# Kernel optimization log

Measured on AMD Instinct MI355X. Metric: run time of the kernel, lower is better.

## Reference

```python
import jax, jax.numpy as jnp
import numpy as np

B, S, D = 4, 4096, 2048
DFF = 4 * D
SKIP = 0.125


def setup_inputs() -> dict:
    key = jax.random.key(0)
    ks = jax.random.split(key, 4)
    s_in = 1.0 / np.sqrt(D).astype(np.float32)
    s_ff = 1.0 / np.sqrt(DFF).astype(np.float32)
    return {
        "x": jax.random.normal(ks[0], (B, S, D), jnp.float32),
        "Wr": jax.random.normal(ks[1], (D, 1), jnp.float32) * s_in,
        "br": jnp.zeros((1,), jnp.float32),
        "W1": jax.random.normal(ks[2], (D, DFF), jnp.float32) * s_in,
        "b1": jnp.zeros((DFF,), jnp.float32),
        "W2": jax.random.normal(ks[3], (DFF, D), jnp.float32) * s_ff,
        "b2": jnp.zeros((D,), jnp.float32),
    }


def reference(x, Wr, br, W1, b1, W2, b2):
    Bs, Ss, Ds = x.shape
    k = max(int(Ss * SKIP), 1)
    # Router: tiny linear D -> 1
    logits = (x @ Wr + br)[..., 0]                      # [B, S]
    # Top-k token selection along sequence
    weights, idx = jax.lax.top_k(logits, k)             # [B, k] (unsorted order within topk)
    perm = jnp.argsort(idx, axis=1)                     # torch.sort's sort-indices
    tokens = jnp.take_along_axis(idx, perm, axis=1)     # sorted token positions [B, k]
    # Gather selected tokens
    fx = jnp.take_along_axis(x, tokens[..., None], axis=1)  # [B, k, D]
    h = jax.nn.gelu(fx @ W1 + b1, approximate=False)    # [B, k, 4D]
    out_l = h @ W2 + b2                                  # [B, k, D]
    # Softmax over topk router logits, reordered to sorted-token order
    tw = jax.nn.softmax(weights, axis=1)                # [B, k]
    rw = jnp.take_along_axis(tw, perm, axis=1)          # [B, k]
    xw = rw[..., None] * out_l                           # [B, k, D]
    # scatter_add back onto x at the selected token positions
    bidx = jnp.arange(Bs)[:, None]                       # [B, 1]
    return x.at[bidx, tokens].add(xw)
```

## Files before the change

kernel.cpp:

```cpp
#include <hip/hip_runtime.h>
#include <math.h>

#define B_DIM   4
#define S_DIM   4096
#define D_DIM   2048
#define DFF_DIM 8192
#define K_TOP   512
#define M_ROWS  (B_DIM * K_TOP)
#define NSPLIT  4

typedef _Float16 half8 __attribute__((ext_vector_type(8)));
typedef _Float16 half4 __attribute__((ext_vector_type(4)));
typedef float    floatx4 __attribute__((ext_vector_type(4)));

static const size_t OFF_LOGITS = 0;
static const size_t OFF_TOK    = 65536;
static const size_t OFF_RW     = 73728;
static const size_t OFF_FX     = 81920;
static const size_t OFF_W1T    = OFF_FX  + (size_t)M_ROWS * D_DIM * 2;
static const size_t OFF_W2T    = OFF_W1T + (size_t)DFF_DIM * D_DIM * 2;
static const size_t OFF_H      = OFF_W2T + (size_t)D_DIM * DFF_DIM * 2;
static const size_t WS_NEEDED  = OFF_H   + (size_t)M_ROWS * DFF_DIM * 2;
static const size_t OFF_PART   = OFF_W1T;

__device__ __forceinline__ void async_ld16(const void* g, void* l) {
  __builtin_amdgcn_global_load_lds((const __attribute__((address_space(1))) unsigned int*)g,
                                   (__attribute__((address_space(3))) unsigned int*)l,
                                   16, 0, 0);
}

__global__ __launch_bounds__(256) void router_logits(const float* __restrict__ x,
                                                     const float* __restrict__ Wr,
                                                     const float* __restrict__ br,
                                                     float* __restrict__ logits) {
  int row  = blockIdx.x * 4 + (threadIdx.x >> 6);
  int lane = threadIdx.x & 63;
  const float4* xr = (const float4*)(x + (size_t)row * D_DIM);
  const float4* wr = (const float4*)Wr;
  float s = 0.f;
#pragma unroll
  for (int i = 0; i < (D_DIM / 4) / 64; ++i) {
    float4 a = xr[lane + i * 64];
    float4 w = wr[lane + i * 64];
    s += a.x * w.x + a.y * w.y + a.z * w.z + a.w * w.w;
  }
#pragma unroll
  for (int off = 32; off > 0; off >>= 1) s += __shfl_down(s, off, 64);
  if (lane == 0) logits[row] = s + br[0];
}

__global__ __launch_bounds__(256) void topk_select(const float* __restrict__ logits,
                                                   int* __restrict__ tokens,
                                                   float* __restrict__ rw) {
  int b = blockIdx.x;
  const float* lg = logits + (size_t)b * S_DIM;
  __shared__ unsigned int keys[S_DIM];
  __shared__ unsigned int bins[256];
  __shared__ unsigned int sscan[256];
  __shared__ unsigned int sh_prefix, sh_r;
  __shared__ float sel_logit[K_TOP];
  __shared__ float red[8];

  int tid = threadIdx.x;
  for (int s = tid; s < S_DIM; s += 256) {
    unsigned int u = __float_as_uint(lg[s]);
    keys[s] = (u & 0x80000000u) ? ~u : (u | 0x80000000u);
  }
  if (tid == 0) { sh_prefix = 0u; sh_r = K_TOP; }
  __syncthreads();

  for (int p = 24; p >= 0; p -= 8) {
    bins[tid] = 0u;
    __syncthreads();
    unsigned int prefix = sh_prefix;
    unsigned int maskhi = (p == 24) ? 0u : (0xFFFFFFFFu << (p + 8));
    for (int s = tid; s < S_DIM; s += 256) {
      unsigned int kk = keys[s];
      if ((kk & maskhi) == prefix) atomicAdd(&bins[(kk >> p) & 255u], 1u);
    }
    __syncthreads();
    sscan[tid] = bins[255 - tid];
    __syncthreads();
#pragma unroll
    for (int off = 1; off < 256; off <<= 1) {
      unsigned int v = (tid >= off) ? sscan[tid - off] : 0u;
      __syncthreads();
      sscan[tid] += v;
      __syncthreads();
    }
    unsigned int r = sh_r;
    unsigned int above = (tid > 0) ? sscan[tid - 1] : 0u;
    bool hit = (sscan[tid] >= r) && (above < r);
    __syncthreads();
    if (hit) {
      sh_prefix = prefix | ((unsigned int)(255 - tid) << p);
      sh_r = r - above;
    }
    __syncthreads();
  }
  unsigned int T = sh_prefix;

  int s0 = tid * 16;
  unsigned int g = 0, e = 0;
#pragma unroll
  for (int j = 0; j < 16; ++j) {
    unsigned int kk = keys[s0 + j];
    g += (kk > T);
    e += (kk == T);
  }
  sscan[tid] = g | (e << 16);
  __syncthreads();
#pragma unroll
  for (int off = 1; off < 256; off <<= 1) {
    unsigned int v = (tid >= off) ? sscan[tid - off] : 0u;
    __syncthreads();
    sscan[tid] += v;
    __syncthreads();
  }
  unsigned int incl = sscan[tid];
  unsigned int Gtot = sscan[255] & 0xFFFFu;
  unsigned int need = (unsigned int)K_TOP - Gtot;
  unsigned int gr = (incl & 0xFFFFu) - g;
  unsigned int er = (incl >> 16) - e;
#pragma unroll
  for (int j = 0; j < 16; ++j) {
    unsigned int kk = keys[s0 + j];
    if (kk > T) {
      unsigned int pos = gr + (er < need ? er : need);
      tokens[b * K_TOP + (int)pos] = s0 + j;
      sel_logit[pos] = __uint_as_float((kk & 0x80000000u) ? (kk & 0x7FFFFFFFu) : ~kk);
      gr++;
    } else if (kk == T) {
      if (er < need) {
        unsigned int pos = gr + er;
        tokens[b * K_TOP + (int)pos] = s0 + j;
        sel_logit[pos] = __uint_as_float((kk & 0x80000000u) ? (kk & 0x7FFFFFFFu) : ~kk);
      }
      er++;
    }
  }
  __syncthreads();

  int lane = tid & 63, wv = tid >> 6;
  float mx = -1e30f;
  for (int i = tid; i < K_TOP; i += 256) mx = fmaxf(mx, sel_logit[i]);
#pragma unroll
  for (int off = 32; off > 0; off >>= 1) mx = fmaxf(mx, __shfl_down(mx, off, 64));
  if (lane == 0) red[wv] = mx;
  __syncthreads();
  if (tid == 0) red[0] = fmaxf(fmaxf(red[0], red[1]), fmaxf(red[2], red[3]));
  __syncthreads();
  float M = red[0];
  float sm = 0.f;
  for (int i = tid; i < K_TOP; i += 256) sm += expf(sel_logit[i] - M);
#pragma unroll
  for (int off = 32; off > 0; off >>= 1) sm += __shfl_down(sm, off, 64);
  if (lane == 0) red[4 + wv] = sm;
  __syncthreads();
  if (tid == 0) red[4] = red[4] + red[5] + red[6] + red[7];
  __syncthreads();
  float SUM = red[4];
  for (int i = tid; i < K_TOP; i += 256) rw[b * K_TOP + i] = expf(sel_logit[i] - M) / SUM;
}

__global__ __launch_bounds__(256) void transpose_cvt(const float* __restrict__ in,
                                                     _Float16* __restrict__ out,
                                                     int K, int N) {
  __shared__ float tile[64][65];
  int nb = blockIdx.x * 64, kb = blockIdx.y * 64;
  int tid = threadIdx.x;
  int lr = tid >> 4;
  int lc = (tid & 15) * 4;
#pragma unroll
  for (int p = 0; p < 4; ++p) {
    int row = p * 16 + lr;
    float4 v = *(const float4*)(in + (size_t)(kb + row) * N + nb + lc);
    tile[row][lc] = v.x; tile[row][lc + 1] = v.y; tile[row][lc + 2] = v.z; tile[row][lc + 3] = v.w;
  }
  __syncthreads();
#pragma unroll
  for (int p = 0; p < 2; ++p) {
    int cc = p * 256 + tid;
    int n  = cc >> 3;
    int kc = (cc & 7) * 8;
    half8 o;
#pragma unroll
    for (int j = 0; j < 8; ++j) o[j] = (_Float16)tile[kc + j][n];
    *(half8*)(out + (size_t)(nb + n) * K + kb + kc) = o;
  }
}

__global__ __launch_bounds__(256) void gather_cvt(const float* __restrict__ x,
                                                  const int* __restrict__ tokens,
                                                  _Float16* __restrict__ fx) {
  int row = blockIdx.x;
  int b = row >> 9;
  int token = tokens[row];
  const float4* src = (const float4*)(x + ((size_t)b * S_DIM + token) * D_DIM);
  half4* dst = (half4*)(fx + (size_t)row * D_DIM);
  for (int i = threadIdx.x; i < D_DIM / 4; i += 256) {
    float4 v = src[i];
    half4 o;
    o[0] = (_Float16)v.x; o[1] = (_Float16)v.y; o[2] = (_Float16)v.z; o[3] = (_Float16)v.w;
    dst[i] = o;
  }
}

template <int EPI>
__global__ __launch_bounds__(256) void gemm_bt(const _Float16* __restrict__ A,
                                               const _Float16* __restrict__ Bt,
                                               const float* __restrict__ bias,
                                               _Float16* __restrict__ Co,
                                               int M, int N, int K, int Kspan) {
  __shared__ _Float16 As[128 * 32];
  __shared__ _Float16 Bs[128 * 32];
  const int tid = threadIdx.x;
  const int lane = tid & 63;
  const int wave = tid >> 6;
  const int bm = blockIdx.y * 128;
  const int bn = blockIdx.x * 128;
  const int wm = (wave & 1) * 64;
  const int wn = (wave >> 1) * 64;
  const int mr = lane & 15;
  const int sw = (((lane >> 4) ^ ((lane >> 1) & 3))) * 8;
  const int k0 = blockIdx.z * Kspan;

  floatx4 acc[4][4] = {};

  for (int kt = k0; kt < k0 + Kspan; kt += 32) {
#pragma unroll
    for (int j = 0; j < 2; ++j) {
      int c = (wave * 2 + j) * 64 + lane;
      int m  = c >> 2;
      int g  = (c & 3) ^ ((m >> 1) & 3);
      async_ld16(A  + (size_t)(bm + m) * K + kt + g * 8, As + (size_t)(wave * 2 + j) * 512);
      async_ld16(Bt + (size_t)(bn + m) * K + kt + g * 8, Bs + (size_t)(wave * 2 + j) * 512);
    }
    __syncthreads();

    half8 af[4], bf[4];
#pragma unroll
    for (int i = 0; i < 4; ++i) af[i] = *(const half8*)(As + (wm + i * 16 + mr) * 32 + sw);
#pragma unroll
    for (int j = 0; j < 4; ++j) bf[j] = *(const half8*)(Bs + (wn + j * 16 + mr) * 32 + sw);
#pragma unroll
    for (int i = 0; i < 4; ++i)
#pragma unroll
      for (int j = 0; j < 4; ++j)
        acc[i][j] = __builtin_amdgcn_mfma_f32_16x16x32_f16(af[i], bf[j], acc[i][j], 0, 0, 0);
    __syncthreads();
  }

  const int r0 = (lane >> 4) * 4;
  const int cn = lane & 15;
  if (EPI == 0) {
#pragma unroll
    for (int i = 0; i < 4; ++i)
#pragma unroll
      for (int j = 0; j < 4; ++j) {
        int col = bn + wn + j * 16 + cn;
        float bv = bias[col];
#pragma unroll
        for (int r = 0; r < 4; ++r) {
          int row = bm + wm + i * 16 + r0 + r;
          float v = acc[i][j][r] + bv;
          v = 0.5f * v * (1.0f + erff(v * 0.7071067811865475f));
          Co[(size_t)row * N + col] = (_Float16)v;
        }
      }
  } else {
    size_t zoff = (size_t)blockIdx.z * M;
#pragma unroll
    for (int i = 0; i < 4; ++i)
#pragma unroll
      for (int j = 0; j < 4; ++j) {
        int col = bn + wn + j * 16 + cn;
#pragma unroll
        for (int r = 0; r < 4; ++r) {
          int row = bm + wm + i * 16 + r0 + r;
          Co[(zoff + row) * N + col] = (_Float16)acc[i][j][r];
        }
      }
  }
}

__global__ __launch_bounds__(256) void reduce_scatter(const _Float16* __restrict__ part,
                                                      const float* __restrict__ bias,
                                                      const int* __restrict__ tokens,
                                                      const float* __restrict__ rw,
                                                      float* __restrict__ out) {
  int m = blockIdx.x;
  int b = m >> 9;
  int token = tokens[m];
  float wgt = rw[m];
  float* orow = out + ((size_t)b * S_DIM + token) * D_DIM;
  int c = threadIdx.x * 8;
  float acc[8] = {0, 0, 0, 0, 0, 0, 0, 0};
#pragma unroll
  for (int kz = 0; kz < NSPLIT; ++kz) {
    half8 p = *(const half8*)(part + ((size_t)kz * M_ROWS + m) * D_DIM + c);
#pragma unroll
    for (int j = 0; j < 8; ++j) acc[j] += (float)p[j];
  }
  float4 o0 = *(const float4*)(orow + c);
  float4 o1 = *(const float4*)(orow + c + 4);
  float4 b0 = *(const float4*)(bias + c);
  float4 b1 = *(const float4*)(bias + c + 4);
  o0.x += wgt * (acc[0] + b0.x);
  o0.y += wgt * (acc[1] + b0.y);
  o0.z += wgt * (acc[2] + b0.z);
  o0.w += wgt * (acc[3] + b0.w);
  o1.x += wgt * (acc[4] + b1.x);
  o1.y += wgt * (acc[5] + b1.y);
  o1.z += wgt * (acc[6] + b1.z);
  o1.w += wgt * (acc[7] + b1.w);
  *(float4*)(orow + c)     = o0;
  *(float4*)(orow + c + 4) = o1;
}

extern "C" void kernel_launch(void* const* d_in, const int* in_sizes, int n_in,
                              void* d_out, int out_size, void* d_ws, size_t ws_size,
                              hipStream_t stream) {
  const float* x  = (const float*)d_in[0];
  const float* Wr = (const float*)d_in[1];
  const float* br = (const float*)d_in[2];
  const float* W1 = (const float*)d_in[3];
  const float* b1 = (const float*)d_in[4];
  const float* W2 = (const float*)d_in[5];
  const float* b2 = (const float*)d_in[6];
  float* out = (float*)d_out;

  if (ws_size < WS_NEEDED) return;

  char* ws = (char*)d_ws;
  float*     logits = (float*)(ws + OFF_LOGITS);
  int*       tokens = (int*)(ws + OFF_TOK);
  float*     rw     = (float*)(ws + OFF_RW);
  _Float16*  fx     = (_Float16*)(ws + OFF_FX);
  _Float16*  W1T    = (_Float16*)(ws + OFF_W1T);
  _Float16*  W2T    = (_Float16*)(ws + OFF_W2T);
  _Float16*  h      = (_Float16*)(ws + OFF_H);
  _Float16*  part   = (_Float16*)(ws + OFF_PART);

  hipMemcpyAsync(out, x, (size_t)B_DIM * S_DIM * D_DIM * sizeof(float),
                 hipMemcpyDeviceToDevice, stream);

  transpose_cvt<<<dim3(DFF_DIM / 64, D_DIM / 64), 256, 0, stream>>>(W1, W1T, D_DIM, DFF_DIM);
  transpose_cvt<<<dim3(D_DIM / 64, DFF_DIM / 64), 256, 0, stream>>>(W2, W2T, DFF_DIM, D_DIM);

  router_logits<<<(B_DIM * S_DIM) / 4, 256, 0, stream>>>(x, Wr, br, logits);
  topk_select<<<B_DIM, 256, 0, stream>>>(logits, tokens, rw);
  gather_cvt<<<M_ROWS, 256, 0, stream>>>(x, tokens, fx);

  gemm_bt<0><<<dim3(DFF_DIM / 128, M_ROWS / 128, 1), 256, 0, stream>>>(
      fx, W1T, b1, h, M_ROWS, DFF_DIM, D_DIM, D_DIM);
  gemm_bt<2><<<dim3(D_DIM / 128, M_ROWS / 128, NSPLIT), 256, 0, stream>>>(
      h, W2T, nullptr, part, M_ROWS, D_DIM, DFF_DIM, DFF_DIM / NSPLIT);
  reduce_scatter<<<M_ROWS, 256, 0, stream>>>(part, b2, tokens, rw, out);
}
```

Measured before the change: 625.6 us.

## Double-buffer GEMM LDS tiles and fuse output copy with scatter-add

The GEMM main loop now uses two LDS buffers with manual s_waitcnt and barriers, so the asynchronous global-to-LDS loads for the next K-tile run while MFMAs consume the current one. The device-to-device memcpy of x into the output and the separate scatter kernel are replaced by one finalize kernel over all tokens. It copies x and, for selected tokens found through a new selmap, adds the weighted FFN result. That selmap reuses the logits workspace region, so it depends on topk_select reading each logit before overwriting it, and the hand-coded waitcnt masks must match the hardware encoding.

```diff
diff --git a/kernel.cpp b/kernel.cpp
--- a/kernel.cpp
+++ b/kernel.cpp
@@ -14,6 +14,7 @@
 typedef float    floatx4 __attribute__((ext_vector_type(4)));
 
 static const size_t OFF_LOGITS = 0;
+static const size_t OFF_SELMAP = 0;
 static const size_t OFF_TOK    = 65536;
 static const size_t OFF_RW     = 73728;
 static const size_t OFF_FX     = 81920;
@@ -28,6 +29,10 @@
                                    (__attribute__((address_space(3))) unsigned int*)l,
                                    16, 0, 0);
 }
+
+#define WAITCNT_VM4   0x0F74
+#define WAITCNT_VM0   0x0F70
+#define WAITCNT_LGKM0 0xC07F
 
 __global__ __launch_bounds__(256) void router_logits(const float* __restrict__ x,
                                                      const float* __restrict__ Wr,
@@ -49,7 +54,8 @@
   if (lane == 0) logits[row] = s + br[0];
 }
 
-__global__ __launch_bounds__(256) void topk_select(const float* __restrict__ logits,
+__global__ __launch_bounds__(256) void topk_select(const float* logits,
+                                                   int* selmap,
                                                    int* __restrict__ tokens,
                                                    float* __restrict__ rw) {
   int b = blockIdx.x;
@@ -65,6 +71,7 @@
   for (int s = tid; s < S_DIM; s += 256) {
     unsigned int u = __float_as_uint(lg[s]);
     keys[s] = (u & 0x80000000u) ? ~u : (u | 0x80000000u);
+    selmap[b * S_DIM + s] = -1;
   }
   if (tid == 0) { sh_prefix = 0u; sh_r = K_TOP; }
   __syncthreads();
@@ -129,12 +136,14 @@
       unsigned int pos = gr + (er < need ? er : need);
       tokens[b * K_TOP + (int)pos] = s0 + j;
       sel_logit[pos] = __uint_as_float((kk & 0x80000000u) ? (kk & 0x7FFFFFFFu) : ~kk);
+      selmap[b * S_DIM + s0 + j] = (int)pos;
       gr++;
     } else if (kk == T) {
       if (er < need) {
         unsigned int pos = gr + er;
         tokens[b * K_TOP + (int)pos] = s0 + j;
         sel_logit[pos] = __uint_as_float((kk & 0x80000000u) ? (kk & 0x7FFFFFFFu) : ~kk);
+        selmap[b * S_DIM + s0 + j] = (int)pos;
       }
       er++;
     }
@@ -212,8 +221,8 @@
                                                const float* __restrict__ bias,
                                                _Float16* __restrict__ Co,
                                                int M, int N, int K, int Kspan) {
-  __shared__ _Float16 As[128 * 32];
-  __shared__ _Float16 Bs[128 * 32];
+  __shared__ _Float16 As[2][128 * 32];
+  __shared__ _Float16 Bs[2][128 * 32];
   const int tid = threadIdx.x;
   const int lane = tid & 63;
   const int wave = tid >> 6;
@@ -222,33 +231,78 @@
   const int wm = (wave & 1) * 64;
   const int wn = (wave >> 1) * 64;
   const int mr = lane & 15;
-  const int sw = (((lane >> 4) ^ ((lane >> 1) & 3))) * 8;
+  const int sw = ((lane >> 4) ^ ((lane >> 1) & 3)) * 8;
   const int k0 = blockIdx.z * Kspan;
+  const int kend = k0 + Kspan;
+
+  const int c0 = (wave * 2) * 64 + lane;
+  const int c1 = (wave * 2 + 1) * 64 + lane;
+  const int m0 = c0 >> 2, g0 = (c0 & 3) ^ ((m0 >> 1) & 3);
+  const int m1 = c1 >> 2, g1 = (c1 & 3) ^ ((m1 >> 1) & 3);
+  const _Float16* a0p = A  + (size_t)(bm + m0) * K + g0 * 8;
+  const _Float16* a1p = A  + (size_t)(bm + m1) * K + g1 * 8;
+  const _Float16* b0p = Bt + (size_t)(bn + m0) * K + g0 * 8;
+  const _Float16* b1p = Bt + (size_t)(bn + m1) * K + g1 * 8;
+  const int slot0 = (wave * 2) * 512;
+  const int slot1 = (wave * 2 + 1) * 512;
 
   floatx4 acc[4][4] = {};
 
-  for (int kt = k0; kt < k0 + Kspan; kt += 32) {
-#pragma unroll
-    for (int j = 0; j < 2; ++j) {
-      int c = (wave * 2 + j) * 64 + lane;
-      int m  = c >> 2;
-      int g  = (c & 3) ^ ((m >> 1) & 3);
-      async_ld16(A  + (size_t)(bm + m) * K + kt + g * 8, As + (size_t)(wave * 2 + j) * 512);
-      async_ld16(Bt + (size_t)(bn + m) * K + kt + g * 8, Bs + (size_t)(wave * 2 + j) * 512);
-    }
-    __syncthreads();
-
-    half8 af[4], bf[4];
-#pragma unroll
-    for (int i = 0; i < 4; ++i) af[i] = *(const half8*)(As + (wm + i * 16 + mr) * 32 + sw);
-#pragma unroll
-    for (int j = 0; j < 4; ++j) bf[j] = *(const half8*)(Bs + (wn + j * 16 + mr) * 32 + sw);
-#pragma unroll
-    for (int i = 0; i < 4; ++i)
-#pragma unroll
-      for (int j = 0; j < 4; ++j)
-        acc[i][j] = __builtin_amdgcn_mfma_f32_16x16x32_f16(af[i], bf[j], acc[i][j], 0, 0, 0);
-    __syncthreads();
+  async_ld16(a0p + k0, &As[0][slot0]);
+  async_ld16(b0p + k0, &Bs[0][slot0]);
+  async_ld16(a1p + k0, &As[0][slot1]);
+  async_ld16(b1p + k0, &Bs[0][slot1]);
+
+  for (int kt = k0; kt < kend; kt += 64) {
+    {
+      int kn = kt + 32;
+      async_ld16(a0p + kn, &As[1][slot0]);
+      async_ld16(b0p + kn, &Bs[1][slot0]);
+      async_ld16(a1p + kn, &As[1][slot1]);
+      async_ld16(b1p + kn, &Bs[1][slot1]);
+      __builtin_amdgcn_s_waitcnt(WAITCNT_VM4);
+    }
+    __builtin_amdgcn_s_barrier();
+    {
+      half8 af[4], bf[4];
+#pragma unroll
+      for (int i = 0; i < 4; ++i) af[i] = *(const half8*)(&As[0][(wm + i * 16 + mr) * 32 + sw]);
+#pragma unroll
+      for (int j = 0; j < 4; ++j) bf[j] = *(const half8*)(&Bs[0][(wn + j * 16 + mr) * 32 + sw]);
+#pragma unroll
+      for (int i = 0; i < 4; ++i)
+#pragma unroll
+        for (int j = 0; j < 4; ++j)
+          acc[i][j] = __builtin_amdgcn_mfma_f32_16x16x32_f16(af[i], bf[j], acc[i][j], 0, 0, 0);
+    }
+    __builtin_amdgcn_s_waitcnt(WAITCNT_LGKM0);
+    __builtin_amdgcn_s_barrier();
+
+    if (kt + 64 < kend) {
+      int kn = kt + 64;
+      async_ld16(a0p + kn, &As[0][slot0]);
+      async_ld16(b0p + kn, &Bs[0][slot0]);
+      async_ld16(a1p + kn, &As[0][slot1]);
+      async_ld16(b1p + kn, &Bs[0][slot1]);
+      __builtin_amdgcn_s_waitcnt(WAITCNT_VM4);
+    } else {
+      __builtin_amdgcn_s_waitcnt(WAITCNT_VM0);
+    }
+    __builtin_amdgcn_s_barrier();
+    {
+      half8 af[4], bf[4];
+#pragma unroll
+      for (int i = 0; i < 4; ++i) af[i] = *(const half8*)(&As[1][(wm + i * 16 + mr) * 32 + sw]);
+#pragma unroll
+      for (int j = 0; j < 4; ++j) bf[j] = *(const half8*)(&Bs[1][(wn + j * 16 + mr) * 32 + sw]);
+#pragma unroll
+      for (int i = 0; i < 4; ++i)
+#pragma unroll
+        for (int j = 0; j < 4; ++j)
+          acc[i][j] = __builtin_amdgcn_mfma_f32_16x16x32_f16(af[i], bf[j], acc[i][j], 0, 0, 0);
+    }
+    __builtin_amdgcn_s_waitcnt(WAITCNT_LGKM0);
+    __builtin_amdgcn_s_barrier();
   }
 
   const int r0 = (lane >> 4) * 4;
@@ -284,38 +338,40 @@
   }
 }
 
-__global__ __launch_bounds__(256) void reduce_scatter(const _Float16* __restrict__ part,
-                                                      const float* __restrict__ bias,
-                                                      const int* __restrict__ tokens,
-                                                      const float* __restrict__ rw,
-                                                      float* __restrict__ out) {
-  int m = blockIdx.x;
-  int b = m >> 9;
-  int token = tokens[m];
-  float wgt = rw[m];
-  float* orow = out + ((size_t)b * S_DIM + token) * D_DIM;
+__global__ __launch_bounds__(256) void finalize(const float* __restrict__ x,
+                                                const _Float16* __restrict__ part,
+                                                const float* __restrict__ bias,
+                                                const int* __restrict__ selmap,
+                                                const float* __restrict__ rw,
+                                                float* __restrict__ out) {
+  int row = blockIdx.x;
+  size_t base = (size_t)row * D_DIM;
+  int sel = selmap[row];
   int c = threadIdx.x * 8;
-  float acc[8] = {0, 0, 0, 0, 0, 0, 0, 0};
-#pragma unroll
-  for (int kz = 0; kz < NSPLIT; ++kz) {
-    half8 p = *(const half8*)(part + ((size_t)kz * M_ROWS + m) * D_DIM + c);
-#pragma unroll
-    for (int j = 0; j < 8; ++j) acc[j] += (float)p[j];
-  }
-  float4 o0 = *(const float4*)(orow + c);
-  float4 o1 = *(const float4*)(orow + c + 4);
-  float4 b0 = *(const float4*)(bias + c);
-  float4 b1 = *(const float4*)(bias + c + 4);
-  o0.x += wgt * (acc[0] + b0.x);
-  o0.y += wgt * (acc[1] + b0.y);
-  o0.z += wgt * (acc[2] + b0.z);
-  o0.w += wgt * (acc[3] + b0.w);
-  o1.x += wgt * (acc[4] + b1.x);
-  o1.y += wgt * (acc[5] + b1.y);
-  o1.z += wgt * (acc[6] + b1.z);
-  o1.w += wgt * (acc[7] + b1.w);
-  *(float4*)(orow + c)     = o0;
-  *(float4*)(orow + c + 4) = o1;
+  float4 o0 = *(const float4*)(x + base + c);
+  float4 o1 = *(const float4*)(x + base + c + 4);
+  if (sel >= 0) {
+    float wgt = rw[sel];
+    float acc[8] = {0, 0, 0, 0, 0, 0, 0, 0};
+#pragma unroll
+    for (int kz = 0; kz < NSPLIT; ++kz) {
+      half8 p = *(const half8*)(part + ((size_t)kz * M_ROWS + sel) * D_DIM + c);
+#pragma unroll
+      for (int j = 0; j < 8; ++j) acc[j] += (float)p[j];
+    }
+    float4 b0 = *(const float4*)(bias + c);
+    float4 b1 = *(const float4*)(bias + c + 4);
+    o0.x += wgt * (acc[0] + b0.x);
+    o0.y += wgt * (acc[1] + b0.y);
+    o0.z += wgt * (acc[2] + b0.z);
+    o0.w += wgt * (acc[3] + b0.w);
+    o1.x += wgt * (acc[4] + b1.x);
+    o1.y += wgt * (acc[5] + b1.y);
+    o1.z += wgt * (acc[6] + b1.z);
+    o1.w += wgt * (acc[7] + b1.w);
+  }
+  *(float4*)(out + base + c)     = o0;
+  *(float4*)(out + base + c + 4) = o1;
 }
 
 extern "C" void kernel_launch(void* const* d_in, const int* in_sizes, int n_in,
@@ -334,6 +390,7 @@
 
   char* ws = (char*)d_ws;
   float*     logits = (float*)(ws + OFF_LOGITS);
+  int*       selmap = (int*)(ws + OFF_SELMAP);
   int*       tokens = (int*)(ws + OFF_TOK);
   float*     rw     = (float*)(ws + OFF_RW);
   _Float16*  fx     = (_Float16*)(ws + OFF_FX);
@@ -342,19 +399,16 @@
   _Float16*  h      = (_Float16*)(ws + OFF_H);
   _Float16*  part   = (_Float16*)(ws + OFF_PART);
 
-  hipMemcpyAsync(out, x, (size_t)B_DIM * S_DIM * D_DIM * sizeof(float),
-                 hipMemcpyDeviceToDevice, stream);
-
   transpose_cvt<<<dim3(DFF_DIM / 64, D_DIM / 64), 256, 0, stream>>>(W1, W1T, D_DIM, DFF_DIM);
   transpose_cvt<<<dim3(D_DIM / 64, DFF_DIM / 64), 256, 0, stream>>>(W2, W2T, DFF_DIM, D_DIM);
 
   router_logits<<<(B_DIM * S_DIM) / 4, 256, 0, stream>>>(x, Wr, br, logits);
-  topk_select<<<B_DIM, 256, 0, stream>>>(logits, tokens, rw);
+  topk_select<<<B_DIM, 256, 0, stream>>>(logits, selmap, tokens, rw);
   gather_cvt<<<M_ROWS, 256, 0, stream>>>(x, tokens, fx);
 
   gemm_bt<0><<<dim3(DFF_DIM / 128, M_ROWS / 128, 1), 256, 0, stream>>>(
       fx, W1T, b1, h, M_ROWS, DFF_DIM, D_DIM, D_DIM);
   gemm_bt<2><<<dim3(D_DIM / 128, M_ROWS / 128, NSPLIT), 256, 0, stream>>>(
       h, W2T, nullptr, part, M_ROWS, D_DIM, DFF_DIM, DFF_DIM / NSPLIT);
-  reduce_scatter<<<M_ROWS, 256, 0, stream>>>(part, b2, tokens, rw, out);
-}
+  finalize<<<B_DIM * S_DIM, 256, 0, stream>>>(x, part, b2, selmap, rw, out);
+}
```

Result: faster. 600.7 us (-4.0%).
